# Optimization experiments

Measured on AMD Instinct MI355X. Metric: run time of the kernel, lower is better.

Reference implementation:

```python
import jax, jax.numpy as jnp
import numpy as np

BN_EPS = 1e-5
DIST_MIN = 1e-10


def _three_nn(p1t, p2t):
    # p1t: [B,N,3], p2t: [B,S,3] -> squared dists/idx of 3 nearest, [B,N,3]
    d2 = (jnp.sum(p1t * p1t, -1, keepdims=True)
          - 2.0 * jnp.einsum('bnc,bsc->bns', p1t, p2t)
          + jnp.sum(p2t * p2t, -1)[:, None, :])  # [B,N,S]
    neg, idx = jax.lax.top_k(-d2, 3)
    return -neg, idx


def _gather_knn(f2t, idx):
    # f2t: [B,S,D], idx: [B,N,3] -> [B,N,3,D]
    return jax.vmap(lambda f, i: f[i])(f2t, idx)


def _conv_bn_relu(x, W, b, g, beta):
    # x: [B,C,N]; 1x1 conv == channel GEMM, then train-mode BN, then ReLU
    y = jnp.einsum('oc,bcn->bon', W, x) + b[None, :, None]
    mean = jnp.mean(y, axis=(0, 2), keepdims=True)
    var = jnp.mean((y - mean) ** 2, axis=(0, 2), keepdims=True)
    yn = (y - mean) * jax.lax.rsqrt(var + BN_EPS)
    return jax.nn.relu(yn * g[None, :, None] + beta[None, :, None])


def setup_inputs() -> dict:
    key = jax.random.key(0)
    ks = jax.random.split(key, 10)
    B, N, S, D1, D2 = 4, 8192, 2048, 128, 256
    C_in, C_mid, C_out = D1 + D2, 256, 256
    inp = {
        'pos1': jax.random.normal(ks[0], (B, 3, N), jnp.float32),
        'pos2': jax.random.normal(ks[1], (B, 3, S), jnp.float32),
        'feature1': jax.random.normal(ks[2], (B, D1, N), jnp.float32),
        'feature2': jax.random.normal(ks[3], (B, D2, S), jnp.float32),
        'W1': jax.random.normal(ks[4], (C_mid, C_in), jnp.float32) / np.sqrt(C_in),
        'b1': jnp.zeros((C_mid,), jnp.float32),
        'g1': jnp.ones((C_mid,), jnp.float32),
        'beta1': jnp.zeros((C_mid,), jnp.float32),
        'W2': jax.random.normal(ks[5], (C_out, C_mid), jnp.float32) / np.sqrt(C_mid),
        'b2': jnp.zeros((C_out,), jnp.float32),
        'g2': jnp.ones((C_out,), jnp.float32),
        'beta2': jnp.zeros((C_out,), jnp.float32),
    }
    return inp


def reference(pos1, pos2, feature1, feature2, W1, b1, g1, beta1, W2, b2, g2, beta2):
    B = pos1.shape[0]
    p1t = jnp.transpose(pos1, (0, 2, 1))  # [B,N,3]
    p2t = jnp.transpose(pos2, (0, 2, 1))  # [B,S,3]
    dists, idx = _three_nn(p1t, p2t)      # [B,N,3]
    dists = jnp.maximum(dists, DIST_MIN)
    w = 1.0 / dists
    w = w / jnp.sum(w, -1, keepdims=True)  # [B,N,3]
    f2t = jnp.transpose(feature2, (0, 2, 1))  # [B,S,D2]
    gathered = _gather_knn(f2t, idx)           # [B,N,3,D2]
    interp = jnp.sum(gathered * w[..., None], axis=2)  # [B,N,D2]
    interp = jnp.transpose(interp, (0, 2, 1))          # [B,D2,N]
    feat = jnp.concatenate([interp, feature1], axis=1)  # [B,D2+D1,N]
    feat = _conv_bn_relu(feat, W1, b1, g1, beta1)
    feat = _conv_bn_relu(feat, W2, b2, g2, beta2)
    return feat
```

## Files before the change

kernel.cpp:

```cpp
#include <hip/hip_runtime.h>
#include <hip/hip_bf16.h>

constexpr int B = 4, N = 8192, S = 2048;

typedef __attribute__((ext_vector_type(8))) short short8;
typedef __attribute__((ext_vector_type(4))) float v4f;

__device__ inline float u2f(ushort u) {
    union { ushort u; __hip_bfloat16 h; } c; c.u = u; return __bfloat162float(c.h);
}
__device__ inline ushort f2u(float f) {
    union { ushort u; __hip_bfloat16 h; } c; c.h = __float2bfloat16(f); return c.u;
}
__device__ inline void async_lds16(const void* g, void* l) {
    __builtin_amdgcn_global_load_lds(
        (const __attribute__((address_space(1))) unsigned*)g,
        (__attribute__((address_space(3))) unsigned*)l, 16, 0, 0);
}
__device__ inline short8 ld8(const ushort* p) { return *(const short8*)p; }

__device__ inline void transpose_tile(
    const float* __restrict__ ip, ushort* __restrict__ op,
    int L, int C, int l0, int c0, int t, ushort (*tl)[66])
{
    const int lr = t & 63, cb = t >> 6;
    #pragma unroll
    for (int i = 0; i < 16; ++i) {
        int c = cb + 4 * i;
        tl[lr][c] = f2u(ip[(size_t)(c0 + c) * L + l0 + lr]);
    }
    __syncthreads();
    const int cp = t & 31, lrow = t >> 5;
    #pragma unroll
    for (int i = 0; i < 8; ++i) {
        int l = lrow + 8 * i;
        ushort2 v;
        v.x = tl[l][2 * cp]; v.y = tl[l][2 * cp + 1];
        *(ushort2*)(op + (size_t)(l0 + l) * C + c0 + 2 * cp) = v;
    }
}

__global__ __launch_bounds__(256) void prep_all(
    const float* __restrict__ W1, const float* __restrict__ W2,
    const float* __restrict__ pos2, const float* __restrict__ f2,
    const float* __restrict__ f1,
    ushort* __restrict__ W1r, ushort* __restrict__ W2r,
    float4* __restrict__ p2pack, float* __restrict__ zero_region,
    ushort* __restrict__ f2T, ushort* __restrict__ f1T)
{
    __shared__ ushort tl[64][66];
    const int bid = blockIdx.x;
    const int t = threadIdx.x;
    if (bid < 512) {
        int b = bid >> 7, ct = (bid >> 5) & 3, st = bid & 31;
        transpose_tile(f2 + (size_t)b * 256 * S, f2T + (size_t)b * S * 256,
                       S, 256, st * 64, ct * 64, t, tl);
    } else if (bid < 1536) {
        int u = bid - 512;
        int b = u >> 8, ct = (u >> 7) & 1, lt = u & 127;
        transpose_tile(f1 + (size_t)b * 128 * N, f1T + (size_t)b * N * 128,
                       N, 128, lt * 64, ct * 64, t, tl);
    } else {
        int i = (bid - 1536) * 256 + t;
        if (i < 12288) {
            int kk = i >> 10, qq = (i >> 8) & 3, o = i & 255;
            const float* src = W1 + o * 384 + kk * 32 + qq * 8;
            float4 a = *(const float4*)src, bb = *(const float4*)(src + 4);
            union { short8 s; ushort u[8]; } pk;
            pk.u[0]=f2u(a.x); pk.u[1]=f2u(a.y); pk.u[2]=f2u(a.z); pk.u[3]=f2u(a.w);
            pk.u[4]=f2u(bb.x); pk.u[5]=f2u(bb.y); pk.u[6]=f2u(bb.z); pk.u[7]=f2u(bb.w);
            *(short8*)(W1r + i * 8) = pk.s;
        } else if (i < 20480) {
            int u = i - 12288;
            int kk = u >> 10, qq = (u >> 8) & 3, o = u & 255;
            const float* src = W2 + o * 256 + kk * 32 + qq * 8;
            float4 a = *(const float4*)src, bb = *(const float4*)(src + 4);
            union { short8 s; ushort u[8]; } pk;
            pk.u[0]=f2u(a.x); pk.u[1]=f2u(a.y); pk.u[2]=f2u(a.z); pk.u[3]=f2u(a.w);
            pk.u[4]=f2u(bb.x); pk.u[5]=f2u(bb.y); pk.u[6]=f2u(bb.z); pk.u[7]=f2u(bb.w);
            *(short8*)(W2r + u * 8) = pk.s;
        } else if (i < 21504) {
            zero_region[i - 20480] = 0.f;
        } else if (i < 21504 + B * S) {
            int u = i - 21504;
            int b = u >> 11, s = u & (S - 1);
            float x = pos2[(b * 3 + 0) * S + s];
            float y = pos2[(b * 3 + 1) * S + s];
            float z = pos2[(b * 3 + 2) * S + s];
            p2pack[u] = make_float4(x, y, z, x * x + y * y + z * z);
        }
    }
}

__global__ __launch_bounds__(512) void knn_gemm1(
    const float* __restrict__ pos1, const float4* __restrict__ p2pack,
    const ushort* __restrict__ W1r, const float* __restrict__ bias1,
    const ushort* __restrict__ f2T, const ushort* __restrict__ f1T,
    ushort* __restrict__ y, float* __restrict__ sums)
{
    __shared__ __align__(16) char smem[81920];
    ushort* Xs   = (ushort*)smem;
    ushort* Wbuf = (ushort*)(smem + 49152);
    float*  dL   = (float*)(smem + 65536);
    int*    iL   = (int*)  (smem + 65536 + 6144);
    float*  wgtL = (float*)(smem + 65536 + 12288);
    int*    idxL = (int*)  (smem + 65536 + 13056);

    const int t = threadIdx.x;
    const int lane = t & 63;
    const int w = __builtin_amdgcn_readfirstlane(t >> 6);
    const int b = blockIdx.y;
    const int n0 = blockIdx.x * 64;
    const int q = lane >> 4, r = lane & 15, r7 = r & 7;

    #pragma unroll
    for (int jj = 0; jj < 2; ++jj)
        async_lds16((const char*)W1r + jj * 8192 + t * 16,
                    (char*)Wbuf + jj * 8192 + w * 1024);

    {
        const int qi = n0 + lane;
        const float x1 = pos1[(b * 3 + 0) * N + qi];
        const float y1 = pos1[(b * 3 + 1) * N + qi];
        const float z1 = pos1[(b * 3 + 2) * N + qi];
        const float t1 = x1 * x1 + y1 * y1 + z1 * z1;
        const float4* __restrict__ pp = p2pack + b * S + w * 256;
        float d0 = 3.4e38f, d1 = 3.4e38f, d2 = 3.4e38f;
        int i0 = 0x7fffffff, i1 = 0x7fffffff, i2 = 0x7fffffff;
        #pragma unroll 8
        for (int i = 0; i < 256; ++i) {
            float4 p = pp[i];
            float dot = fmaf(x1, p.x, fmaf(y1, p.y, z1 * p.z));
            float dd = fmaf(-2.f, dot, t1) + p.w;
            int s = w * 256 + i;
            bool c0 = dd < d0, c1 = dd < d1, c2 = dd < d2;
            i2 = c1 ? i1 : (c2 ? s : i2);
            i1 = c0 ? i0 : (c1 ? s : i1);
            i0 = c0 ? s : i0;
            float nd1 = __builtin_amdgcn_fmed3f(dd, d0, d1);
            float nd2 = __builtin_amdgcn_fmed3f(dd, d1, d2);
            d0 = fminf(d0, dd);
            d1 = nd1; d2 = nd2;
        }
        int base = (w * 64 + lane) * 3;
        dL[base + 0] = d0; dL[base + 1] = d1; dL[base + 2] = d2;
        iL[base + 0] = i0; iL[base + 1] = i1; iL[base + 2] = i2;
    }
    __syncthreads();
    if (t < 64) {
        float f0 = dL[t*3+0], fv1 = dL[t*3+1], fv2 = dL[t*3+2];
        int   j0 = iL[t*3+0], j1 = iL[t*3+1], j2 = iL[t*3+2];
        #pragma unroll
        for (int c = 1; c < 8; ++c) {
            int cb = (c * 64 + t) * 3;
            #pragma unroll
            for (int k = 0; k < 3; ++k) {
                float d = dL[cb + k]; int id = iL[cb + k];
                bool l0 = (d < f0)  || (d == f0  && id < j0);
                bool l1 = (d < fv1) || (d == fv1 && id < j1);
                bool l2 = (d < fv2) || (d == fv2 && id < j2);
                if (l0)      { fv2 = fv1; j2 = j1; fv1 = f0; j1 = j0; f0 = d; j0 = id; }
                else if (l1) { fv2 = fv1; j2 = j1; fv1 = d; j1 = id; }
                else if (l2) { fv2 = d; j2 = id; }
            }
        }
        float w0 = 1.f / fmaxf(f0, 1e-10f);
        float w1 = 1.f / fmaxf(fv1, 1e-10f);
        float w2 = 1.f / fmaxf(fv2, 1e-10f);
        float inv = 1.f / (w0 + w1 + w2);
        j0 = ((unsigned)j0 < S) ? j0 : 0;
        j1 = ((unsigned)j1 < S) ? j1 : 0;
        j2 = ((unsigned)j2 < S) ? j2 : 0;
        wgtL[t*3+0] = w0 * inv; wgtL[t*3+1] = w1 * inv; wgtL[t*3+2] = w2 * inv;
        idxL[t*3+0] = j0; idxL[t*3+1] = j1; idxL[t*3+2] = j2;
    }
    __syncthreads();

    {
        const int lp = t & 31, ro = t >> 5;
        #pragma unroll
        for (int it = 0; it < 4; ++it) {
            int rr = ro + 16 * it;
            int s0 = idxL[rr*3+0], s1 = idxL[rr*3+1], s2 = idxL[rr*3+2];
            float w0 = wgtL[rr*3+0], w1 = wgtL[rr*3+1], w2 = wgtL[rr*3+2];
            union { short8 s; ushort u[8]; } a, c, d, o;
            a.s = ld8(f2T + ((size_t)b * S + s0) * 256 + 8 * lp);
            c.s = ld8(f2T + ((size_t)b * S + s1) * 256 + 8 * lp);
            d.s = ld8(f2T + ((size_t)b * S + s2) * 256 + 8 * lp);
            #pragma unroll
            for (int j = 0; j < 8; ++j)
                o.u[j] = f2u(w0 * u2f(a.u[j]) + w1 * u2f(c.u[j]) + w2 * u2f(d.u[j]));
            *(short8*)(Xs + rr * 384 + ((lp ^ (rr & 7)) * 8)) = o.s;
        }
    }
    {
        const int lp = t & 15, ro = t >> 4;
        #pragma unroll
        for (int it = 0; it < 2; ++it) {
            int rr = ro + 32 * it;
            short8 v = ld8(f1T + ((size_t)b * N + n0 + rr) * 128 + 8 * lp);
            int c = 32 + lp;
            *(short8*)(Xs + rr * 384 + ((c ^ (rr & 7)) * 8)) = v;
        }
    }
    __syncthreads();

    v4f acc[2][4];
    #pragma unroll
    for (int mt = 0; mt < 2; ++mt)
        #pragma unroll
        for (int nf = 0; nf < 4; ++nf) acc[mt][nf] = (v4f){0.f, 0.f, 0.f, 0.f};

    for (int kk = 0; kk < 12; ++kk) {
        if (kk < 11) {
            const char* g = (const char*)W1r + (kk + 1) * 16384;
            char* l = (char*)Wbuf + ((kk + 1) & 1) * 16384;
            #pragma unroll
            for (int jj = 0; jj < 2; ++jj)
                async_lds16(g + jj * 8192 + t * 16, l + jj * 8192 + w * 1024);
        }
        const ushort* Wb = Wbuf + (kk & 1) * 8192;
        short8 af[2], bf[4];
        #pragma unroll
        for (int mt = 0; mt < 2; ++mt)
            af[mt] = ld8(Wb + q * 2048 + (w * 32 + mt * 16 + r) * 8);
        #pragma unroll
        for (int nf = 0; nf < 4; ++nf)
            bf[nf] = ld8(Xs + (nf * 16 + r) * 384 + (((kk * 4 + q) ^ r7) * 8));
        #pragma unroll
        for (int mt = 0; mt < 2; ++mt)
            #pragma unroll
            for (int nf = 0; nf < 4; ++nf)
                acc[mt][nf] = __builtin_amdgcn_mfma_f32_16x16x32_bf16(
                    af[mt], bf[nf], acc[mt][nf], 0, 0, 0);
        __syncthreads();
    }

    float* statS = (float*)Xs;
    float* statQ = statS + 256;
    #pragma unroll
    for (int mt = 0; mt < 2; ++mt) {
        int ob = w * 32 + mt * 16 + q * 4;
        float4 bi = *(const float4*)(bias1 + ob);
        float sj0 = 0, sj1 = 0, sj2 = 0, sj3 = 0;
        float qj0 = 0, qj1 = 0, qj2 = 0, qj3 = 0;
        #pragma unroll
        for (int nf = 0; nf < 4; ++nf) {
            int n = n0 + nf * 16 + r;
            float v0 = acc[mt][nf][0] + bi.x, v1 = acc[mt][nf][1] + bi.y;
            float v2 = acc[mt][nf][2] + bi.z, v3 = acc[mt][nf][3] + bi.w;
            ushort4 pk; pk.x = f2u(v0); pk.y = f2u(v1); pk.z = f2u(v2); pk.w = f2u(v3);
            *(ushort4*)(y + ((size_t)b * N + n) * 256 + ob) = pk;
            sj0 += v0; sj1 += v1; sj2 += v2; sj3 += v3;
            qj0 += v0 * v0; qj1 += v1 * v1; qj2 += v2 * v2; qj3 += v3 * v3;
        }
        #pragma unroll
        for (int m = 1; m <= 8; m <<= 1) {
            sj0 += __shfl_xor(sj0, m); sj1 += __shfl_xor(sj1, m);
            sj2 += __shfl_xor(sj2, m); sj3 += __shfl_xor(sj3, m);
            qj0 += __shfl_xor(qj0, m); qj1 += __shfl_xor(qj1, m);
            qj2 += __shfl_xor(qj2, m); qj3 += __shfl_xor(qj3, m);
        }
        if (r == 0) {
            statS[ob + 0] = sj0; statS[ob + 1] = sj1;
            statS[ob + 2] = sj2; statS[ob + 3] = sj3;
            statQ[ob + 0] = qj0; statQ[ob + 1] = qj1;
            statQ[ob + 2] = qj2; statQ[ob + 3] = qj3;
        }
    }
    __syncthreads();
    if (t < 256) {
        atomicAdd(&sums[t], statS[t]);
        atomicAdd(&sums[256 + t], statQ[t]);
    }
}

__global__ __launch_bounds__(512) void gemm2_kernel(
    const ushort* __restrict__ Wr, const float* __restrict__ bias,
    const float* __restrict__ sums1, const float* __restrict__ g1,
    const float* __restrict__ be1,
    ushort* __restrict__ y, float* __restrict__ sums)
{
    __shared__ __align__(16) ushort Xs[64 * 256];
    __shared__ __align__(16) ushort Wbuf[2 * 8192];
    __shared__ float ssA[256], ssB[256];
    const int t = threadIdx.x;
    const int b = blockIdx.y;
    const int n0 = blockIdx.x * 64;
    const int w = t >> 6, lane = t & 63;
    const int q = lane >> 4, r = lane & 15, r7 = r & 7;

    {
        const char* g0 = (const char*)Wr;
        #pragma unroll
        for (int jj = 0; jj < 2; ++jj)
            async_lds16(g0 + jj * 8192 + t * 16,
                        (char*)Wbuf + jj * 8192 + w * 1024);
    }

    if (t < 256) {
        float sv = sums1[t], qv = sums1[256 + t];
        float mean = sv * (1.f / 32768.f);
        float var = qv * (1.f / 32768.f) - mean * mean;
        float rstd = rsqrtf(var + 1e-5f);
        float sc = g1[t] * rstd;
        ssA[t] = sc;
        ssB[t] = be1[t] - mean * sc;
    }
    __syncthreads();

    {
        const int lp = t & 31, ro = t >> 5;
        #pragma unroll
        for (int it = 0; it < 4; ++it) {
            int rr = ro + 16 * it;
            union { short8 s; ushort u[8]; } v, o;
            v.s = ld8(y + ((size_t)b * N + n0 + rr) * 256 + 8 * lp);
            #pragma unroll
            for (int j = 0; j < 8; ++j)
                o.u[j] = f2u(fmaxf(u2f(v.u[j]) * ssA[8 * lp + j] + ssB[8 * lp + j], 0.f));
            *(short8*)(Xs + rr * 256 + ((lp ^ (rr & 7)) * 8)) = o.s;
        }
    }
    __syncthreads();

    v4f acc[2][4];
    #pragma unroll
    for (int mt = 0; mt < 2; ++mt)
        #pragma unroll
        for (int nf = 0; nf < 4; ++nf) acc[mt][nf] = (v4f){0.f, 0.f, 0.f, 0.f};

    for (int kk = 0; kk < 8; ++kk) {
        if (kk < 7) {
            const char* g = (const char*)Wr + (kk + 1) * 16384;
            char* l = (char*)Wbuf + ((kk + 1) & 1) * 16384;
            #pragma unroll
            for (int jj = 0; jj < 2; ++jj)
                async_lds16(g + jj * 8192 + t * 16, l + jj * 8192 + w * 1024);
        }
        const ushort* Wb = Wbuf + (kk & 1) * 8192;
        short8 af[2], bf[4];
        #pragma unroll
        for (int mt = 0; mt < 2; ++mt)
            af[mt] = ld8(Wb + q * 2048 + (w * 32 + mt * 16 + r) * 8);
        #pragma unroll
        for (int nf = 0; nf < 4; ++nf)
            bf[nf] = ld8(Xs + (nf * 16 + r) * 256 + (((kk * 4 + q) ^ r7) * 8));
        #pragma unroll
        for (int mt = 0; mt < 2; ++mt)
            #pragma unroll
            for (int nf = 0; nf < 4; ++nf)
                acc[mt][nf] = __builtin_amdgcn_mfma_f32_16x16x32_bf16(
                    af[mt], bf[nf], acc[mt][nf], 0, 0, 0);
        __syncthreads();
    }

    float* statS = (float*)Xs;
    float* statQ = statS + 256;
    #pragma unroll
    for (int mt = 0; mt < 2; ++mt) {
        int ob = w * 32 + mt * 16 + q * 4;
        float4 bi = *(const float4*)(bias + ob);
        float sj0 = 0, sj1 = 0, sj2 = 0, sj3 = 0;
        float qj0 = 0, qj1 = 0, qj2 = 0, qj3 = 0;
        #pragma unroll
        for (int nf = 0; nf < 4; ++nf) {
            int n = n0 + nf * 16 + r;
            float v0 = acc[mt][nf][0] + bi.x, v1 = acc[mt][nf][1] + bi.y;
            float v2 = acc[mt][nf][2] + bi.z, v3 = acc[mt][nf][3] + bi.w;
            ushort4 pk; pk.x = f2u(v0); pk.y = f2u(v1); pk.z = f2u(v2); pk.w = f2u(v3);
            *(ushort4*)(y + ((size_t)b * N + n) * 256 + ob) = pk;
            sj0 += v0; sj1 += v1; sj2 += v2; sj3 += v3;
            qj0 += v0 * v0; qj1 += v1 * v1; qj2 += v2 * v2; qj3 += v3 * v3;
        }
        #pragma unroll
        for (int m = 1; m <= 8; m <<= 1) {
            sj0 += __shfl_xor(sj0, m); sj1 += __shfl_xor(sj1, m);
            sj2 += __shfl_xor(sj2, m); sj3 += __shfl_xor(sj3, m);
            qj0 += __shfl_xor(qj0, m); qj1 += __shfl_xor(qj1, m);
            qj2 += __shfl_xor(qj2, m); qj3 += __shfl_xor(qj3, m);
        }
        if (r == 0) {
            statS[ob + 0] = sj0; statS[ob + 1] = sj1;
            statS[ob + 2] = sj2; statS[ob + 3] = sj3;
            statQ[ob + 0] = qj0; statQ[ob + 1] = qj1;
            statQ[ob + 2] = qj2; statQ[ob + 3] = qj3;
        }
    }
    __syncthreads();
    if (t < 256) {
        atomicAdd(&sums[t], statS[t]);
        atomicAdd(&sums[256 + t], statQ[t]);
    }
}

__global__ __launch_bounds__(256) void final_kernel(
    const ushort* __restrict__ Y, const float* __restrict__ sums2,
    const float* __restrict__ g2, const float* __restrict__ be2,
    float* __restrict__ out)
{
    __shared__ float tl[64][65];
    __shared__ float ssA[64], ssB[64];
    const int t = threadIdx.x;
    const int b = blockIdx.z;
    const int n0 = blockIdx.x * 64, c0 = blockIdx.y * 64;

    if (t < 64) {
        int c = c0 + t;
        float sv = sums2[c], qv = sums2[256 + c];
        float mean = sv * (1.f / 32768.f);
        float var = qv * (1.f / 32768.f) - mean * mean;
        float rstd = rsqrtf(var + 1e-5f);
        float sc = g2[c] * rstd;
        ssA[t] = sc;
        ssB[t] = be2[c] - mean * sc;
    }
    __syncthreads();

    const int nl = t >> 3, cho = 8 * (t & 7);
    #pragma unroll
    for (int it = 0; it < 2; ++it) {
        int n = nl + 32 * it;
        union { short8 s; ushort u[8]; } v;
        v.s = ld8(Y + ((size_t)b * N + n0 + n) * 256 + c0 + cho);
        #pragma unroll
        for (int j = 0; j < 8; ++j)
            tl[n][cho + j] = fmaxf(u2f(v.u[j]) * ssA[cho + j] + ssB[cho + j], 0.f);
    }
    __syncthreads();

    const int cl = t >> 4, n4 = (t & 15) * 4;
    #pragma unroll
    for (int it = 0; it < 4; ++it) {
        int c = cl + 16 * it;
        float4 v;
        v.x = tl[n4 + 0][c]; v.y = tl[n4 + 1][c];
        v.z = tl[n4 + 2][c]; v.w = tl[n4 + 3][c];
        *(float4*)(out + ((size_t)b * 256 + c0 + c) * N + n0 + n4) = v;
    }
}

extern "C" void kernel_launch(void* const* d_in, const int* in_sizes, int n_in,
                              void* d_out, int out_size, void* d_ws, size_t ws_size,
                              hipStream_t stream)
{
    (void)in_sizes; (void)n_in; (void)out_size;
    if (ws_size < (30u << 20)) return;

    const float* pos1 = (const float*)d_in[0];
    const float* pos2 = (const float*)d_in[1];
    const float* f1   = (const float*)d_in[2];
    const float* f2   = (const float*)d_in[3];
    const float* W1   = (const float*)d_in[4];
    const float* b1   = (const float*)d_in[5];
    const float* g1   = (const float*)d_in[6];
    const float* be1  = (const float*)d_in[7];
    const float* W2   = (const float*)d_in[8];
    const float* b2   = (const float*)d_in[9];
    const float* g2   = (const float*)d_in[10];
    const float* be2  = (const float*)d_in[11];

    char* ws = (char*)d_ws;
    float*  sums1  = (float*)ws;
    float*  sums2  = sums1 + 512;
    ushort* W1r    = (ushort*)(ws + 4096);
    ushort* W2r    = (ushort*)(ws + 4096 + 196608);
    float4* p2pack = (float4*)(ws + 4096 + 196608 + 131072);
    ushort* f2T    = (ushort*)(ws + (1u << 19));
    ushort* f1T    = (ushort*)(ws + (1u << 19) + (4u << 20));
    ushort* y      = (ushort*)(ws + (1u << 19) + (12u << 20));

    prep_all<<<1652, 256, 0, stream>>>(W1, W2, pos2, f2, f1,
                                       W1r, W2r, p2pack, sums1, f2T, f1T);

    knn_gemm1<<<dim3(N / 64, B), 512, 0, stream>>>(
        pos1, p2pack, W1r, b1, f2T, f1T, y, sums1);

    gemm2_kernel<<<dim3(N / 64, B), 512, 0, stream>>>(
        W2r, b2, sums1, g1, be1, y, sums2);

    final_kernel<<<dim3(N / 64, 256 / 64, B), 256, 0, stream>>>(
        y, sums2, g2, be2, (float*)d_out);
}
```

Baseline: 185.1 us.

## Move 3-NN search into prep kernel to overlap with transposes

The three-nearest-neighbour search moves from the GEMM1 kernel into the prep kernel, where it runs concurrently with the feature transposes and weight packing. Each KNN block stages pos2 packed into LDS instead of reading a global p2pack buffer, and writes indices and weights to global memory for GEMM1 to read. Prep blocks grow to 512 threads, with two transpose tiles per block. The aim is to take the KNN latency off the GEMM1 critical path, at the cost of an extra global round trip for indices and weights.

After: 185.7 us. Within noise of the previous version (+0.4%).

```diff
diff --git a/kernel.cpp b/kernel.cpp
--- a/kernel.cpp
+++ b/kernel.cpp
@@ -21,16 +21,16 @@
 
 __device__ inline void transpose_tile(
     const float* __restrict__ ip, ushort* __restrict__ op,
-    int L, int C, int l0, int c0, int t, ushort (*tl)[66])
+    int L, int C, int l0, int c0, int tt, ushort (*tl)[66])
 {
-    const int lr = t & 63, cb = t >> 6;
+    const int lr = tt & 63, cb = tt >> 6;
     #pragma unroll
     for (int i = 0; i < 16; ++i) {
         int c = cb + 4 * i;
         tl[lr][c] = f2u(ip[(size_t)(c0 + c) * L + l0 + lr]);
     }
     __syncthreads();
-    const int cp = t & 31, lrow = t >> 5;
+    const int cp = tt & 31, lrow = tt >> 5;
     #pragma unroll
     for (int i = 0; i < 8; ++i) {
         int l = lrow + 8 * i;
@@ -40,71 +40,140 @@
     }
 }
 
-__global__ __launch_bounds__(256) void prep_all(
+__global__ __launch_bounds__(512) void prep_all(
     const float* __restrict__ W1, const float* __restrict__ W2,
     const float* __restrict__ pos2, const float* __restrict__ f2,
-    const float* __restrict__ f1,
+    const float* __restrict__ f1, const float* __restrict__ pos1,
     ushort* __restrict__ W1r, ushort* __restrict__ W2r,
-    float4* __restrict__ p2pack, float* __restrict__ zero_region,
-    ushort* __restrict__ f2T, ushort* __restrict__ f1T)
+    float* __restrict__ zero_region,
+    ushort* __restrict__ f2T, ushort* __restrict__ f1T,
+    float* __restrict__ wgt, int* __restrict__ idxb)
 {
-    __shared__ ushort tl[64][66];
+    __shared__ __align__(16) char sm[45056];
     const int bid = blockIdx.x;
     const int t = threadIdx.x;
+
     if (bid < 512) {
-        int b = bid >> 7, ct = (bid >> 5) & 3, st = bid & 31;
+        float4* pk = (float4*)sm;
+        float*  dL = (float*)(sm + 32768);
+        int*    iL = (int*)  (sm + 32768 + 6144);
+        const int b = bid >> 7, n0 = (bid & 127) * 64;
+        const int lane = t & 63;
+        const int w = __builtin_amdgcn_readfirstlane(t >> 6);
+
+        for (int i = t; i < S; i += 512) {
+            float x = pos2[(b * 3 + 0) * S + i];
+            float y = pos2[(b * 3 + 1) * S + i];
+            float z = pos2[(b * 3 + 2) * S + i];
+            pk[i] = make_float4(x, y, z, x * x + y * y + z * z);
+        }
+        __syncthreads();
+
+        {
+            const int qi = n0 + lane;
+            const float x1 = pos1[(b * 3 + 0) * N + qi];
+            const float y1 = pos1[(b * 3 + 1) * N + qi];
+            const float z1 = pos1[(b * 3 + 2) * N + qi];
+            const float t1 = x1 * x1 + y1 * y1 + z1 * z1;
+            const float4* __restrict__ pp = pk + w * 256;
+            float d0 = 3.4e38f, d1 = 3.4e38f, d2 = 3.4e38f;
+            int i0 = 0x7fffffff, i1 = 0x7fffffff, i2 = 0x7fffffff;
+            #pragma unroll 8
+            for (int i = 0; i < 256; ++i) {
+                float4 p = pp[i];
+                float dot = fmaf(x1, p.x, fmaf(y1, p.y, z1 * p.z));
+                float dd = fmaf(-2.f, dot, t1) + p.w;
+                int s = w * 256 + i;
+                bool c0 = dd < d0, c1 = dd < d1, c2 = dd < d2;
+                i2 = c1 ? i1 : (c2 ? s : i2);
+                i1 = c0 ? i0 : (c1 ? s : i1);
+                i0 = c0 ? s : i0;
+                float nd1 = __builtin_amdgcn_fmed3f(dd, d0, d1);
+                float nd2 = __builtin_amdgcn_fmed3f(dd, d1, d2);
+                d0 = fminf(d0, dd);
+                d1 = nd1; d2 = nd2;
+            }
+            int base = (w * 64 + lane) * 3;
+            dL[base + 0] = d0; dL[base + 1] = d1; dL[base + 2] = d2;
+            iL[base + 0] = i0; iL[base + 1] = i1; iL[base + 2] = i2;
+        }
+        __syncthreads();
+        if (t < 64) {
+            float f0 = dL[t*3+0], fv1 = dL[t*3+1], fv2 = dL[t*3+2];
+            int   j0 = iL[t*3+0], j1 = iL[t*3+1], j2 = iL[t*3+2];
+            #pragma unroll
+            for (int c = 1; c < 8; ++c) {
+                int cb = (c * 64 + t) * 3;
+                #pragma unroll
+                for (int k = 0; k < 3; ++k) {
+                    float d = dL[cb + k]; int id = iL[cb + k];
+                    bool l0 = (d < f0)  || (d == f0  && id < j0);
+                    bool l1 = (d < fv1) || (d == fv1 && id < j1);
+                    bool l2 = (d < fv2) || (d == fv2 && id < j2);
+                    if (l0)      { fv2 = fv1; j2 = j1; fv1 = f0; j1 = j0; f0 = d; j0 = id; }
+                    else if (l1) { fv2 = fv1; j2 = j1; fv1 = d; j1 = id; }
+                    else if (l2) { fv2 = d; j2 = id; }
+                }
+            }
+            float w0 = 1.f / fmaxf(f0, 1e-10f);
+            float w1 = 1.f / fmaxf(fv1, 1e-10f);
+            float w2 = 1.f / fmaxf(fv2, 1e-10f);
+            float inv = 1.f / (w0 + w1 + w2);
+            j0 = ((unsigned)j0 < S) ? j0 : 0;
+            j1 = ((unsigned)j1 < S) ? j1 : 0;
+            j2 = ((unsigned)j2 < S) ? j2 : 0;
+            int base = (b * N + n0 + t) * 3;
+            wgt[base + 0] = w0 * inv; wgt[base + 1] = w1 * inv; wgt[base + 2] = w2 * inv;
+            idxb[base + 0] = j0; idxb[base + 1] = j1; idxb[base + 2] = j2;
+        }
+    } else if (bid < 768) {
+        ushort (*tl)[66] = (ushort(*)[66])(sm + (t >> 8) * 16896);
+        const int tt = t & 255;
+        int tile = (bid - 512) * 2 + (t >> 8);
+        int b = tile >> 7, ct = (tile >> 5) & 3, st = tile & 31;
         transpose_tile(f2 + (size_t)b * 256 * S, f2T + (size_t)b * S * 256,
-                       S, 256, st * 64, ct * 64, t, tl);
-    } else if (bid < 1536) {
-        int u = bid - 512;
+                       S, 256, st * 64, ct * 64, tt, tl);
+    } else if (bid < 1280) {
+        ushort (*tl)[66] = (ushort(*)[66])(sm + (t >> 8) * 16896);
+        const int tt = t & 255;
+        int u = (bid - 768) * 2 + (t >> 8);
         int b = u >> 8, ct = (u >> 7) & 1, lt = u & 127;
         transpose_tile(f1 + (size_t)b * 128 * N, f1T + (size_t)b * N * 128,
-                       N, 128, lt * 64, ct * 64, t, tl);
+                       N, 128, lt * 64, ct * 64, tt, tl);
     } else {
-        int i = (bid - 1536) * 256 + t;
+        int i = (bid - 1280) * 512 + t;
         if (i < 12288) {
             int kk = i >> 10, qq = (i >> 8) & 3, o = i & 255;
             const float* src = W1 + o * 384 + kk * 32 + qq * 8;
             float4 a = *(const float4*)src, bb = *(const float4*)(src + 4);
-            union { short8 s; ushort u[8]; } pk;
-            pk.u[0]=f2u(a.x); pk.u[1]=f2u(a.y); pk.u[2]=f2u(a.z); pk.u[3]=f2u(a.w);
-            pk.u[4]=f2u(bb.x); pk.u[5]=f2u(bb.y); pk.u[6]=f2u(bb.z); pk.u[7]=f2u(bb.w);
-            *(short8*)(W1r + i * 8) = pk.s;
+            union { short8 s; ushort u[8]; } pkv;
+            pkv.u[0]=f2u(a.x); pkv.u[1]=f2u(a.y); pkv.u[2]=f2u(a.z); pkv.u[3]=f2u(a.w);
+            pkv.u[4]=f2u(bb.x); pkv.u[5]=f2u(bb.y); pkv.u[6]=f2u(bb.z); pkv.u[7]=f2u(bb.w);
+            *(short8*)(W1r + i * 8) = pkv.s;
         } else if (i < 20480) {
             int u = i - 12288;
             int kk = u >> 10, qq = (u >> 8) & 3, o = u & 255;
             const float* src = W2 + o * 256 + kk * 32 + qq * 8;
             float4 a = *(const float4*)src, bb = *(const float4*)(src + 4);
-            union { short8 s; ushort u[8]; } pk;
-            pk.u[0]=f2u(a.x); pk.u[1]=f2u(a.y); pk.u[2]=f2u(a.z); pk.u[3]=f2u(a.w);
-            pk.u[4]=f2u(bb.x); pk.u[5]=f2u(bb.y); pk.u[6]=f2u(bb.z); pk.u[7]=f2u(bb.w);
-            *(short8*)(W2r + u * 8) = pk.s;
+            union { short8 s; ushort u[8]; } pkv;
+            pkv.u[0]=f2u(a.x); pkv.u[1]=f2u(a.y); pkv.u[2]=f2u(a.z); pkv.u[3]=f2u(a.w);
+            pkv.u[4]=f2u(bb.x); pkv.u[5]=f2u(bb.y); pkv.u[6]=f2u(bb.z); pkv.u[7]=f2u(bb.w);
+            *(short8*)(W2r + u * 8) = pkv.s;
         } else if (i < 21504) {
             zero_region[i - 20480] = 0.f;
-        } else if (i < 21504 + B * S) {
-            int u = i - 21504;
-            int b = u >> 11, s = u & (S - 1);
-            float x = pos2[(b * 3 + 0) * S + s];
-            float y = pos2[(b * 3 + 1) * S + s];
-            float z = pos2[(b * 3 + 2) * S + s];
-            p2pack[u] = make_float4(x, y, z, x * x + y * y + z * z);
-        }
-    }
-}
-
-__global__ __launch_bounds__(512) void knn_gemm1(
-    const float* __restrict__ pos1, const float4* __restrict__ p2pack,
+        }
+    }
+}
+
+__global__ __launch_bounds__(512) void gemm1_kernel(
     const ushort* __restrict__ W1r, const float* __restrict__ bias1,
     const ushort* __restrict__ f2T, const ushort* __restrict__ f1T,
+    const int* __restrict__ idxb, const float* __restrict__ wgt,
     ushort* __restrict__ y, float* __restrict__ sums)
 {
     __shared__ __align__(16) char smem[81920];
     ushort* Xs   = (ushort*)smem;
     ushort* Wbuf = (ushort*)(smem + 49152);
-    float*  dL   = (float*)(smem + 65536);
-    int*    iL   = (int*)  (smem + 65536 + 6144);
-    float*  wgtL = (float*)(smem + 65536 + 12288);
-    int*    idxL = (int*)  (smem + 65536 + 13056);
 
     const int t = threadIdx.x;
     const int lane = t & 63;
@@ -119,70 +188,16 @@
                     (char*)Wbuf + jj * 8192 + w * 1024);
 
     {
-        const int qi = n0 + lane;
-        const float x1 = pos1[(b * 3 + 0) * N + qi];
-        const float y1 = pos1[(b * 3 + 1) * N + qi];
-        const float z1 = pos1[(b * 3 + 2) * N + qi];
-        const float t1 = x1 * x1 + y1 * y1 + z1 * z1;
-        const float4* __restrict__ pp = p2pack + b * S + w * 256;
-        float d0 = 3.4e38f, d1 = 3.4e38f, d2 = 3.4e38f;
-        int i0 = 0x7fffffff, i1 = 0x7fffffff, i2 = 0x7fffffff;
-        #pragma unroll 8
-        for (int i = 0; i < 256; ++i) {
-            float4 p = pp[i];
-            float dot = fmaf(x1, p.x, fmaf(y1, p.y, z1 * p.z));
-            float dd = fmaf(-2.f, dot, t1) + p.w;
-            int s = w * 256 + i;
-            bool c0 = dd < d0, c1 = dd < d1, c2 = dd < d2;
-            i2 = c1 ? i1 : (c2 ? s : i2);
-            i1 = c0 ? i0 : (c1 ? s : i1);
-            i0 = c0 ? s : i0;
-            float nd1 = __builtin_amdgcn_fmed3f(dd, d0, d1);
-            float nd2 = __builtin_amdgcn_fmed3f(dd, d1, d2);
-            d0 = fminf(d0, dd);
-            d1 = nd1; d2 = nd2;
-        }
-        int base = (w * 64 + lane) * 3;
-        dL[base + 0] = d0; dL[base + 1] = d1; dL[base + 2] = d2;
-        iL[base + 0] = i0; iL[base + 1] = i1; iL[base + 2] = i2;
-    }
-    __syncthreads();
-    if (t < 64) {
-        float f0 = dL[t*3+0], fv1 = dL[t*3+1], fv2 = dL[t*3+2];
-        int   j0 = iL[t*3+0], j1 = iL[t*3+1], j2 = iL[t*3+2];
-        #pragma unroll
-        for (int c = 1; c < 8; ++c) {
-            int cb = (c * 64 + t) * 3;
-            #pragma unroll
-            for (int k = 0; k < 3; ++k) {
-                float d = dL[cb + k]; int id = iL[cb + k];
-                bool l0 = (d < f0)  || (d == f0  && id < j0);
-                bool l1 = (d < fv1) || (d == fv1 && id < j1);
-                bool l2 = (d < fv2) || (d == fv2 && id < j2);
-                if (l0)      { fv2 = fv1; j2 = j1; fv1 = f0; j1 = j0; f0 = d; j0 = id; }
-                else if (l1) { fv2 = fv1; j2 = j1; fv1 = d; j1 = id; }
-                else if (l2) { fv2 = d; j2 = id; }
-            }
-        }
-        float w0 = 1.f / fmaxf(f0, 1e-10f);
-        float w1 = 1.f / fmaxf(fv1, 1e-10f);
-        float w2 = 1.f / fmaxf(fv2, 1e-10f);
-        float inv = 1.f / (w0 + w1 + w2);
-        j0 = ((unsigned)j0 < S) ? j0 : 0;
-        j1 = ((unsigned)j1 < S) ? j1 : 0;
-        j2 = ((unsigned)j2 < S) ? j2 : 0;
-        wgtL[t*3+0] = w0 * inv; wgtL[t*3+1] = w1 * inv; wgtL[t*3+2] = w2 * inv;
-        idxL[t*3+0] = j0; idxL[t*3+1] = j1; idxL[t*3+2] = j2;
-    }
-    __syncthreads();
-
-    {
         const int lp = t & 31, ro = t >> 5;
         #pragma unroll
         for (int it = 0; it < 4; ++it) {
             int rr = ro + 16 * it;
-            int s0 = idxL[rr*3+0], s1 = idxL[rr*3+1], s2 = idxL[rr*3+2];
-            float w0 = wgtL[rr*3+0], w1 = wgtL[rr*3+1], w2 = wgtL[rr*3+2];
+            int base = (b * N + n0 + rr) * 3;
+            int s0 = idxb[base], s1 = idxb[base + 1], s2 = idxb[base + 2];
+            s0 = ((unsigned)s0 < S) ? s0 : 0;
+            s1 = ((unsigned)s1 < S) ? s1 : 0;
+            s2 = ((unsigned)s2 < S) ? s2 : 0;
+            float w0 = wgt[base], w1 = wgt[base + 1], w2 = wgt[base + 2];
             union { short8 s; ushort u[8]; } a, c, d, o;
             a.s = ld8(f2T + ((size_t)b * S + s0) * 256 + 8 * lp);
             c.s = ld8(f2T + ((size_t)b * S + s1) * 256 + 8 * lp);
@@ -463,18 +478,19 @@
     char* ws = (char*)d_ws;
     float*  sums1  = (float*)ws;
     float*  sums2  = sums1 + 512;
-    ushort* W1r    = (ushort*)(ws + 4096);
-    ushort* W2r    = (ushort*)(ws + 4096 + 196608);
-    float4* p2pack = (float4*)(ws + 4096 + 196608 + 131072);
-    ushort* f2T    = (ushort*)(ws + (1u << 19));
-    ushort* f1T    = (ushort*)(ws + (1u << 19) + (4u << 20));
-    ushort* y      = (ushort*)(ws + (1u << 19) + (12u << 20));
-
-    prep_all<<<1652, 256, 0, stream>>>(W1, W2, pos2, f2, f1,
-                                       W1r, W2r, p2pack, sums1, f2T, f1T);
-
-    knn_gemm1<<<dim3(N / 64, B), 512, 0, stream>>>(
-        pos1, p2pack, W1r, b1, f2T, f1T, y, sums1);
+    int*    idxb   = (int*)(ws + 4096);
+    float*  wgt    = (float*)(ws + 4096 + 393216);
+    ushort* W1r    = (ushort*)(ws + 4096 + 786432);
+    ushort* W2r    = (ushort*)(ws + 4096 + 786432 + 196608);
+    ushort* f2T    = (ushort*)(ws + (2u << 20));
+    ushort* f1T    = (ushort*)(ws + (6u << 20));
+    ushort* y      = (ushort*)(ws + (14u << 20));
+
+    prep_all<<<1322, 512, 0, stream>>>(W1, W2, pos2, f2, f1, pos1,
+                                       W1r, W2r, sums1, f2T, f1T, wgt, idxb);
+
+    gemm1_kernel<<<dim3(N / 64, B), 512, 0, stream>>>(
+        W1r, b1, f2T, f1T, idxb, wgt, y, sums1);
 
     gemm2_kernel<<<dim3(N / 64, B), 512, 0, stream>>>(
         W2r, b2, sums1, g1, be1, y, sums2);
```
